# Kernel optimization log

Measured on AMD Instinct MI355X. Metric: run time of the kernel, lower is better.

The kernel has to match this reference:

```python
import jax, jax.numpy as jnp
import numpy as np
import math

S, HID = 2048, 2048
NH, Q_LORA, KV_LORA = 16, 1536, 512
NOPE, ROPE, VDIM = 128, 64, 128
HEAD = NOPE + ROPE  # 192
BLK = 128
EPS = 1e-6
MSCALE = 0.1 * 1.0 * math.log(40.0) + 1.0
SOFTMAX_SCALE = HEAD ** -0.5 * MSCALE * MSCALE


def _dequant(w, s, blk=BLK):
    # w: [out,in] stored quantized values, s: [ceil(out/blk), ceil(in/blk)] block scale_inv
    so = jnp.repeat(s, blk, axis=0)[: w.shape[0]]
    se = jnp.repeat(so, blk, axis=1)[:, : w.shape[1]]
    return w * se


def _mm_dq(x, w, s):
    # mm_w8a16_dq_forward: x @ dequant(w).T
    return x @ _dequant(w, s).T


def _rmsnorm(x, w, eps=EPS):
    var = jnp.mean(x * x, axis=-1, keepdims=True)
    return x * jax.lax.rsqrt(var + eps) * w


def _rotate_half(x):
    h = x.shape[-1] // 2
    return jnp.concatenate([-x[..., h:], x[..., :h]], axis=-1)


def setup_inputs() -> dict:
    key = jax.random.key(0)
    ks = jax.random.split(key, 16)
    d = {
        'hidden_states': jax.random.normal(ks[0], (S, HID), jnp.float32),
        'wq_a': jax.random.normal(ks[1], (Q_LORA, HID), jnp.float32),
        'sq_a': jax.random.uniform(ks[2], (12, 16), jnp.float32) * 0.02 + 0.005,
        'wq_b': jax.random.normal(ks[3], (NH * HEAD, Q_LORA), jnp.float32),
        'sq_b': jax.random.uniform(ks[4], (24, 12), jnp.float32) * 0.02 + 0.005,
        'wkv_a': jax.random.normal(ks[5], (KV_LORA + ROPE, HID), jnp.float32),
        'skv_a': jax.random.uniform(ks[6], (5, 16), jnp.float32) * 0.02 + 0.005,
        'wkv_b': jax.random.normal(ks[7], (NH * (NOPE + VDIM), KV_LORA), jnp.float32),
        'skv_b': jax.random.uniform(ks[8], (32, 4), jnp.float32) * 0.02 + 0.005,
        'wo': jax.random.normal(ks[9], (HID, NH * VDIM), jnp.float32),
        'so': jax.random.uniform(ks[10], (16, 16), jnp.float32) * 0.02 + 0.005,
        'q_ln_w': jnp.ones((Q_LORA,), jnp.float32),
        'kv_ln_w': jnp.ones((KV_LORA,), jnp.float32),
    }
    pos = jnp.arange(S, dtype=jnp.float32)[:, None]
    inv = 1.0 / (10000.0 ** (jnp.arange(0, ROPE, 2, dtype=jnp.float32) / ROPE))
    ang = pos * inv[None, :]
    ang = jnp.concatenate([ang, ang], axis=-1)  # [S, 64]
    d['cos'] = jnp.cos(ang)
    d['sin'] = jnp.sin(ang)
    return d


def reference(hidden_states, cos, sin, wq_a, sq_a, wq_b, sq_b, wkv_a, skv_a,
              wkv_b, skv_b, wo, so, q_ln_w, kv_ln_w):
    # Q low-rank path: q_a -> rmsnorm -> q_b
    lq = _mm_dq(hidden_states, wq_a, sq_a)                 # [S, q_lora]
    q = _mm_dq(_rmsnorm(lq, q_ln_w), wq_b, sq_b)           # [S, NH*HEAD]
    q = q.reshape(S, NH, HEAD)
    q_nope, q_pe = q[..., :NOPE], q[..., NOPE:]            # [S,NH,128], [S,NH,64]

    # KV low-rank + MQA rope path
    lkv = _mm_dq(hidden_states, wkv_a, skv_a)              # [S, kv_lora+rope]
    kv_nope = _rmsnorm(lkv[:, :KV_LORA], kv_ln_w)          # [S, kv_lora]
    k_pe = lkv[:, KV_LORA:]                                # [S, 64] (shared across heads)
    kvb = _mm_dq(kv_nope, wkv_b, skv_b).reshape(S, NH, NOPE + VDIM)
    k_nope, v = kvb[..., :NOPE], kvb[..., NOPE:]           # [S,NH,128] each

    # RoPE (rotate-half) on the pe parts
    q_pe = q_pe * cos[:, None, :] + _rotate_half(q_pe) * sin[:, None, :]
    k_pe = k_pe * cos + _rotate_half(k_pe) * sin           # [S, 64]

    # prefill MLA attention with causal mask
    scores = (jnp.einsum('shd,thd->hst', q_nope, k_nope)
              + jnp.einsum('shd,td->hst', q_pe, k_pe)) * SOFTMAX_SCALE
    causal = jnp.tril(jnp.ones((S, S), bool))
    scores = jnp.where(causal[None], scores, -jnp.inf)
    probs = jax.nn.softmax(scores, axis=-1)                # [NH,S,S]
    attn = jnp.einsum('hst,thd->shd', probs, v).reshape(S, NH * VDIM)

    return _mm_dq(attn, wo, so)                            # [S, HID]
```

## Files before the change

### kernel.cpp

```cpp
#include <hip/hip_runtime.h>

typedef unsigned short u16;
typedef unsigned int u32;
typedef __attribute__((ext_vector_type(8))) short bf16x8;
typedef __attribute__((ext_vector_type(4))) float f32x4;
typedef __attribute__((ext_vector_type(16))) float f32x16;
typedef __attribute__((ext_vector_type(4))) unsigned short u16x4;

#define S_LEN 2048
#define HIDDEN 2048
#define NHEAD 16
#define QLORA 1536
#define KVLORA 512
#define NOPE_D 128
#define ROPE_D 64
#define V_D 128
#define HEAD_D 192
#define NCOMB 2176
#define LOG2E 1.442695041f

__device__ __constant__ float SM_SCALE_C = (float)(0.07216878364870323 *
    ((0.1 * 3.6888794541139363 + 1.0) * (0.1 * 3.6888794541139363 + 1.0)));

__device__ inline u16 f2bf(float f) {
    union { float f; unsigned int u; } v; v.f = f;
    unsigned int r = v.u + 0x7FFFu + ((v.u >> 16) & 1u);
    return (u16)(r >> 16);
}
__device__ inline float bf2f(u16 b) {
    union { unsigned int u; float f; } v; v.u = ((unsigned int)b) << 16;
    return v.f;
}
__device__ inline void gload_lds16(const u16* g, u16* l) {
    __builtin_amdgcn_global_load_lds(
        (const __attribute__((address_space(1))) void*)g,
        (__attribute__((address_space(3))) void*)l, 16, 0, 0);
}

__global__ __launch_bounds__(64)
void prep_weights(const float* __restrict__ hs,
                  const float* __restrict__ wq_a, const float* __restrict__ sq_a,
                  const float* __restrict__ wq_b, const float* __restrict__ sq_b,
                  const float* __restrict__ wkv_a, const float* __restrict__ skv_a,
                  const float* __restrict__ wkv_b, const float* __restrict__ skv_b,
                  const float* __restrict__ wo, const float* __restrict__ so,
                  u16* __restrict__ hs_bf, u16* __restrict__ wcomb,
                  u16* __restrict__ wqb_bf, u16* __restrict__ wkvb_bf,
                  u16* __restrict__ wo_bf) {
    int r = blockIdx.x;
    const float* W; const float* Sc; u16* out; int K, sc_cols, n;
    if (r < 2048)                      { n = r;                     W = hs;    Sc = 0;     out = hs_bf;   K = 2048; sc_cols = 0; }
    else if (r < 2048 + 1536)          { n = r - 2048;              W = wq_a;  Sc = sq_a;  out = wcomb;   K = 2048; sc_cols = 16; }
    else if (r < 2048 + 1536 + 576)    { n = r - (2048 + 1536);     W = wkv_a; Sc = skv_a; out = wcomb + (size_t)QLORA * 2048; K = 2048; sc_cols = 16; }
    else if (r < 2048 + 1536 + 576 + 3072) { n = r - (2048 + 1536 + 576); W = wq_b; Sc = sq_b; out = wqb_bf; K = 1536; sc_cols = 12; }
    else if (r < 2048 + 1536 + 576 + 3072 + 4096) { n = r - (2048 + 1536 + 576 + 3072); W = wkv_b; Sc = skv_b; out = wkvb_bf; K = 512; sc_cols = 4; }
    else                               { n = r - (2048 + 1536 + 576 + 3072 + 4096); W = wo; Sc = so; out = wo_bf; K = 2048; sc_cols = 16; }
    for (int k = threadIdx.x * 8; k < K; k += 512) {
        float sc = Sc ? Sc[(n >> 7) * sc_cols + (k >> 7)] : 1.0f;
        f32x4 v0 = *(const f32x4*)(W + (size_t)n * K + k);
        f32x4 v1 = *(const f32x4*)(W + (size_t)n * K + k + 4);
        bf16x8 o;
        #pragma unroll
        for (int i = 0; i < 4; ++i) {
            o[i]     = (short)f2bf(v0[i] * sc);
            o[i + 4] = (short)f2bf(v1[i] * sc);
        }
        *(bf16x8*)(out + (size_t)n * K + k) = o;
    }
}

__device__ __forceinline__ void gemm_core(
    const u16* __restrict__ A, const u16* __restrict__ W, void* __restrict__ C,
    int M, int N, int Ktot, int Ksub, int mode, int bm, int bn, int bz,
    u16* As, u16* Ws) {
    const int tid = threadIdx.x;
    const int lane = tid & 63;
    const int wv = tid >> 6;
    const int wm = wv >> 1, wn = wv & 1;
    const int lr = lane & 15, lk = lane >> 4;
    const int srow = lane >> 3;
    const int schunk = lane & 7;

    f32x4 acc[4][4] = {};

    const int kbeg = bz * Ksub;
    const int kend = kbeg + Ksub;
    for (int k0 = kbeg; k0 < kend; k0 += 64) {
        __syncthreads();
        #pragma unroll
        for (int i = 0; i < 4; ++i) {
            int t = (wv * 4 + i) * 8 + srow;
            int cs = (schunk ^ (t & 7)) << 3;
            gload_lds16(A + (size_t)(bm + t) * Ktot + k0 + cs, &As[(wv * 4 + i) * 512]);
            gload_lds16(W + (size_t)(bn + t) * Ktot + k0 + cs, &Ws[(wv * 4 + i) * 512]);
        }
        __syncthreads();
        #pragma unroll
        for (int kh = 0; kh < 2; ++kh) {
            bf16x8 af[4], bfr[4];
            #pragma unroll
            for (int mi = 0; mi < 4; ++mi) {
                int r = wm * 64 + mi * 16 + lr;
                af[mi] = *(const bf16x8*)&As[r * 64 + (((kh * 4 + lk) ^ (lr & 7)) << 3)];
            }
            #pragma unroll
            for (int ni = 0; ni < 4; ++ni) {
                int r = wn * 64 + ni * 16 + lr;
                bfr[ni] = *(const bf16x8*)&Ws[r * 64 + (((kh * 4 + lk) ^ (lr & 7)) << 3)];
            }
            #pragma unroll
            for (int mi = 0; mi < 4; ++mi)
                #pragma unroll
                for (int ni = 0; ni < 4; ++ni)
                    acc[mi][ni] = __builtin_amdgcn_mfma_f32_16x16x32_bf16(af[mi], bfr[ni], acc[mi][ni], 0, 0, 0);
        }
    }

    float* Pf = (mode == 2) ? ((float*)C + (size_t)bz * M * N) : (float*)C;
    #pragma unroll
    for (int mi = 0; mi < 4; ++mi)
        #pragma unroll
        for (int ni = 0; ni < 4; ++ni)
            #pragma unroll
            for (int j = 0; j < 4; ++j) {
                int r = bm + wm * 64 + mi * 16 + lk * 4 + j;
                int c = bn + wn * 64 + ni * 16 + lr;
                if (c < N) {
                    if (mode == 1) ((u16*)C)[(size_t)r * N + c] = f2bf(acc[mi][ni][j]);
                    else           Pf[(size_t)r * N + c] = acc[mi][ni][j];
                }
            }
}

__device__ __forceinline__ int xcd_swizzle(int orig, int nwg) {
    int qq = nwg >> 3, rr = nwg & 7, xcd = orig & 7, loc = orig >> 3;
    return (xcd < rr) ? (xcd * (qq + 1) + loc)
                      : (rr * (qq + 1) + (xcd - rr) * qq + loc);
}

__global__ __launch_bounds__(256)
void gemm_bf16(const u16* __restrict__ A, const u16* __restrict__ W,
               void* __restrict__ C, int M, int N, int Ktot, int Ksub, int mode) {
    __shared__ u16 As[128 * 64];
    __shared__ u16 Ws[128 * 64];
    const int gx = gridDim.x, gy = gridDim.y;
    const int nwg = gx * gy * gridDim.z;
    const int orig = blockIdx.x + gx * (blockIdx.y + gy * blockIdx.z);
    const int wg = xcd_swizzle(orig, nwg);
    const int bn = (wg % gx) * 128;
    const int bm = ((wg / gx) % gy) * 128;
    const int bz = wg / (gx * gy);
    gemm_core(A, W, C, M, N, Ktot, Ksub, mode, bm, bn, bz, As, Ws);
}

__global__ __launch_bounds__(256)
void gemm_qh_kvb(const u16* __restrict__ lqn, const u16* __restrict__ wqb, float* __restrict__ arena,
                 const u16* __restrict__ kvn, const u16* __restrict__ wkvb, u16* __restrict__ kvb) {
    __shared__ u16 As[128 * 64];
    __shared__ u16 Ws[128 * 64];
    const int NWG = 24 * 16 * 3 + 32 * 16;
    const int wg = xcd_swizzle(blockIdx.x, NWG);
    if (wg < 24 * 16 * 3) {
        const int bn = (wg % 24) * 128;
        const int bm = ((wg / 24) % 16) * 128;
        const int bz = wg / (24 * 16);
        gemm_core(lqn, wqb, arena, S_LEN, NHEAD * HEAD_D, QLORA, 512, 2, bm, bn, bz, As, Ws);
    } else {
        const int w2 = wg - 24 * 16 * 3;
        const int bn = (w2 % 32) * 128;
        const int bm = (w2 / 32) * 128;
        gemm_core(kvn, wkvb, kvb, S_LEN, NHEAD * 256, KVLORA, 512, 1, bm, bn, 0, As, Ws);
    }
}

__global__ __launch_bounds__(256)
void reduce_rms_comb(const float* __restrict__ P,
                     const float* __restrict__ q_ln, const float* __restrict__ kv_ln,
                     u16* __restrict__ lqn, u16* __restrict__ kvn, u16* __restrict__ kpe) {
    __shared__ float vbuf[NCOMB];
    __shared__ float r2[2][4];
    const int row = blockIdx.x;
    const float* p0 = P + (size_t)row * NCOMB;
    const size_t st = (size_t)S_LEN * NCOMB;
    float ssq = 0.f, ssk = 0.f;
    for (int c = threadIdx.x * 4; c < NCOMB; c += 1024) {
        f32x4 v = *(const f32x4*)(p0 + c);
        v += *(const f32x4*)(p0 + st + c);
        v += *(const f32x4*)(p0 + 2 * st + c);
        v += *(const f32x4*)(p0 + 3 * st + c);
        *(f32x4*)&vbuf[c] = v;
        float s = v[0] * v[0] + v[1] * v[1] + v[2] * v[2] + v[3] * v[3];
        if (c < QLORA) ssq += s;
        else if (c < QLORA + KVLORA) ssk += s;
    }
    #pragma unroll
    for (int off = 1; off < 64; off <<= 1) {
        ssq += __shfl_xor(ssq, off, 64);
        ssk += __shfl_xor(ssk, off, 64);
    }
    if ((threadIdx.x & 63) == 0) {
        r2[0][threadIdx.x >> 6] = ssq;
        r2[1][threadIdx.x >> 6] = ssk;
    }
    __syncthreads();
    float rsq = rsqrtf((r2[0][0] + r2[0][1] + r2[0][2] + r2[0][3]) / (float)QLORA + 1e-6f);
    float rsk = rsqrtf((r2[1][0] + r2[1][1] + r2[1][2] + r2[1][3]) / (float)KVLORA + 1e-6f);
    for (int c = threadIdx.x * 4; c < NCOMB; c += 1024) {
        f32x4 v = *(const f32x4*)&vbuf[c];
        u16x4 o;
        if (c < QLORA) {
            #pragma unroll
            for (int j = 0; j < 4; ++j) o[j] = f2bf(v[j] * rsq * q_ln[c + j]);
            *(u16x4*)(lqn + (size_t)row * QLORA + c) = o;
        } else if (c < QLORA + KVLORA) {
            int cc = c - QLORA;
            #pragma unroll
            for (int j = 0; j < 4; ++j) o[j] = f2bf(v[j] * rsk * kv_ln[cc + j]);
            *(u16x4*)(kvn + (size_t)row * KVLORA + cc) = o;
        } else if (c < QLORA + KVLORA + ROPE_D) {
            int cc = c - QLORA - KVLORA;
            #pragma unroll
            for (int j = 0; j < 4; ++j) o[j] = f2bf(v[j]);
            *(u16x4*)(kpe + (size_t)row * ROPE_D + cc) = o;
        }
    }
}

__global__ __launch_bounds__(256)
void prep_q_frag_red(const float* __restrict__ P, const float* __restrict__ cosb,
                     const float* __restrict__ sinb, u16* __restrict__ qfrag) {
    const int sblk = blockIdx.x, h = blockIdx.y;
    const float sm = SM_SCALE_C;
    const size_t st = (size_t)S_LEN * (NHEAD * HEAD_D);
    #pragma unroll
    for (int c = 0; c < 3; ++c) {
        int idx = c * 256 + threadIdx.x;
        int kk = idx >> 6;
        int lane = idx & 63;
        int s = sblk * 32 + (lane & 31);
        int d0 = kk * 16 + (lane >> 5) * 8;
        const float* p0 = P + (size_t)s * (NHEAD * HEAD_D) + h * HEAD_D;
        bf16x8 o;
        if (d0 < NOPE_D) {
            f32x4 a0 = *(const f32x4*)(p0 + d0) + *(const f32x4*)(p0 + st + d0) + *(const f32x4*)(p0 + 2 * st + d0);
            f32x4 a1 = *(const f32x4*)(p0 + d0 + 4) + *(const f32x4*)(p0 + st + d0 + 4) + *(const f32x4*)(p0 + 2 * st + d0 + 4);
            #pragma unroll
            for (int j = 0; j < 4; ++j) {
                o[j]     = (short)f2bf(a0[j] * sm);
                o[j + 4] = (short)f2bf(a1[j] * sm);
            }
        } else {
            int r0 = d0 - NOPE_D;
            int rp = (r0 + 32) & 63;
            f32x4 x0 = *(const f32x4*)(p0 + d0) + *(const f32x4*)(p0 + st + d0) + *(const f32x4*)(p0 + 2 * st + d0);
            f32x4 x1 = *(const f32x4*)(p0 + d0 + 4) + *(const f32x4*)(p0 + st + d0 + 4) + *(const f32x4*)(p0 + 2 * st + d0 + 4);
            f32x4 r0v = *(const f32x4*)(p0 + NOPE_D + rp) + *(const f32x4*)(p0 + st + NOPE_D + rp) + *(const f32x4*)(p0 + 2 * st + NOPE_D + rp);
            f32x4 r1v = *(const f32x4*)(p0 + NOPE_D + rp + 4) + *(const f32x4*)(p0 + st + NOPE_D + rp + 4) + *(const f32x4*)(p0 + 2 * st + NOPE_D + rp + 4);
            float x[8], rv[8];
            #pragma unroll
            for (int j = 0; j < 4; ++j) { x[j] = x0[j]; x[j + 4] = x1[j]; rv[j] = r0v[j]; rv[j + 4] = r1v[j]; }
            float sign = (r0 < 32) ? -1.f : 1.f;
            #pragma unroll
            for (int j = 0; j < 8; ++j) {
                float cs = cosb[s * ROPE_D + r0 + j];
                float sn = sinb[s * ROPE_D + r0 + j];
                o[j] = (short)f2bf((x[j] * cs + sign * rv[j] * sn) * sm);
            }
        }
        *(bf16x8*)(qfrag + (((size_t)h * 64 + sblk) * 12 + kk) * 512 + lane * 8) = o;
    }
}

__global__ void reduce_out(const float* __restrict__ P, float* __restrict__ out, int n) {
    int i = (blockIdx.x * blockDim.x + threadIdx.x) * 4;
    if (i >= n) return;
    f32x4 v = *(const f32x4*)(P + i);
    v += *(const f32x4*)(P + (size_t)n + i);
    v += *(const f32x4*)(P + 2 * (size_t)n + i);
    v += *(const f32x4*)(P + 3 * (size_t)n + i);
    *(f32x4*)(out + i) = v;
}

__global__ __launch_bounds__(256)
void prep_kv_frag(const u16* __restrict__ kvb, const u16* __restrict__ kpe,
                  const float* __restrict__ cosb, const float* __restrict__ sinb,
                  u16* __restrict__ kfrag, u16* __restrict__ vfrag) {
    __shared__ u16 Vs[32][136];
    const int sblk = blockIdx.x, h = blockIdx.y;
    #pragma unroll
    for (int it = 0; it < 2; ++it) {
        int idx = it * 256 + threadIdx.x;
        int r = idx >> 4;
        int c8 = (idx & 15) * 8;
        int s = sblk * 32 + r;
        *(bf16x8*)&Vs[r][c8] = *(const bf16x8*)(kvb + (size_t)s * (NHEAD * 256) + h * 256 + NOPE_D + c8);
    }
    #pragma unroll
    for (int c = 0; c < 3; ++c) {
        int idx = c * 256 + threadIdx.x;
        int kk = idx >> 6;
        int lane = idx & 63;
        int s = sblk * 32 + (lane & 31);
        int d0 = kk * 16 + (lane >> 5) * 8;
        bf16x8 o;
        if (d0 < NOPE_D) {
            o = *(const bf16x8*)(kvb + (size_t)s * (NHEAD * 256) + h * 256 + d0);
        } else {
            int r0 = d0 - NOPE_D;
            const u16* kp = kpe + (size_t)s * ROPE_D;
            bf16x8 x = *(const bf16x8*)(kp + r0);
            bf16x8 rv = *(const bf16x8*)(kp + ((r0 + 32) & 63));
            float sign = (r0 < 32) ? -1.f : 1.f;
            #pragma unroll
            for (int j = 0; j < 8; ++j) {
                float cs = cosb[s * ROPE_D + r0 + j];
                float sn = sinb[s * ROPE_D + r0 + j];
                o[j] = (short)f2bf(bf2f((u16)x[j]) * cs + sign * bf2f((u16)rv[j]) * sn);
            }
        }
        *(bf16x8*)(kfrag + (((size_t)h * 64 + sblk) * 12 + kk) * 512 + lane * 8) = o;
    }
    __syncthreads();
    #pragma unroll
    for (int it = 0; it < 2; ++it) {
        int idx = it * 256 + threadIdx.x;
        int fi = idx >> 6;
        int lane = idx & 63;
        int bb = fi >> 1, h16 = fi & 1;
        int col = bb * 32 + (lane & 31);
        int row0 = h16 * 16 + (lane >> 5) * 8;
        bf16x8 o;
        #pragma unroll
        for (int j = 0; j < 8; ++j) o[j] = (short)Vs[row0 + j][col];
        *(bf16x8*)(vfrag + (((size_t)h * 64 + sblk) * 8 + fi) * 512 + lane * 8) = o;
    }
}

__global__ __launch_bounds__(256, 2)
void flash_attn4(const u16* __restrict__ qfrag, const u16* __restrict__ kfrag,
                 const u16* __restrict__ vfrag, u16* __restrict__ attn) {
    __shared__ float OB[3][128][32];
    __shared__ float MB[3][2][32];

    const int tid = threadIdx.x, lane = tid & 63, wq = tid >> 6;
    const int b = blockIdx.x;
    const int t = 63 - (b >> 4);
    const int h = ((b & 7) << 1) | ((b >> 3) & 1);
    const int q0 = t * 32;
    const int lq = lane & 31;
    const int hi = lane >> 5;

    const int n = t + 1;
    const int s_lo = (wq * n) >> 2;
    const int s_hi = ((wq + 1) * n) >> 2;

    bf16x8 qfr[12];
    {
        const u16* qb = qfrag + (((size_t)h * 64 + t) * 12) * 512 + lane * 8;
        #pragma unroll
        for (int kk = 0; kk < 12; ++kk) qfr[kk] = *(const bf16x8*)(qb + kk * 512);
    }

    const u16* kfb = kfrag + ((size_t)h * 64 * 12) * 512 + lane * 8;
    const u16* vfb = vfrag + ((size_t)h * 64 * 8) * 512 + lane * 8;

    f32x16 oa[4] = {};
    float mrun = -3.0e38f, lrun = 0.f;

    bf16x8 kcur[12];
    {
        int psub = (s_lo < s_hi) ? s_lo : 0;
        const u16* kp = kfb + (size_t)psub * 12 * 512;
        #pragma unroll
        for (int kk = 0; kk < 12; ++kk)
            kcur[kk] = *(const bf16x8*)(kp + kk * 512);
    }

    for (int sub = s_lo; sub < s_hi; ++sub) {
        f32x16 s0 = {}, s1 = {};
        __builtin_amdgcn_s_setprio(1);
        #pragma unroll
        for (int kk = 0; kk < 12; kk += 2) {
            s0 = __builtin_amdgcn_mfma_f32_32x32x16_bf16(kcur[kk], qfr[kk], s0, 0, 0, 0);
            s1 = __builtin_amdgcn_mfma_f32_32x32x16_bf16(kcur[kk + 1], qfr[kk + 1], s1, 0, 0, 0);
        }
        __builtin_amdgcn_s_setprio(0);
        {
            int nsub = (sub + 1 < s_hi) ? sub + 1 : sub;
            const u16* kp = kfb + (size_t)nsub * 12 * 512;
            #pragma unroll
            for (int kk = 0; kk < 12; ++kk)
                kcur[kk] = *(const bf16x8*)(kp + kk * 512);
        }
        bf16x8 va[8];
        {
            const u16* vp = vfb + (size_t)sub * 8 * 512;
            #pragma unroll
            for (int fi = 0; fi < 8; ++fi)
                va[fi] = *(const bf16x8*)(vp + fi * 512);
        }
        f32x16 sv = s0 + s1;
        if (sub == t) {
            #pragma unroll
            for (int r = 0; r < 16; ++r) {
                int krow = (r & 3) + 8 * (r >> 2) + 4 * hi;
                if (krow > lq) sv[r] = -3.0e38f;
            }
        }
        float tm = sv[0];
        #pragma unroll
        for (int r = 1; r < 16; ++r) tm = fmaxf(tm, sv[r]);
        tm = fmaxf(tm, __shfl_xor(tm, 32, 64));
        if (!__all(tm - mrun <= 8.f)) {
            float mn = fmaxf(mrun, tm);
            float scl = exp2f((mrun - mn) * LOG2E);
            mrun = mn;
            lrun *= scl;
            #pragma unroll
            for (int bb = 0; bb < 4; ++bb)
                #pragma unroll
                for (int r = 0; r < 16; ++r) oa[bb][r] *= scl;
        }
        float p[16];
        float psum = 0.f;
        #pragma unroll
        for (int r = 0; r < 16; ++r) {
            p[r] = exp2f((sv[r] - mrun) * LOG2E);
            psum += p[r];
        }
        psum += __shfl_xor(psum, 32, 64);
        lrun += psum;
        u32 pw[8], sw[8];
        #pragma unroll
        for (int i = 0; i < 8; ++i)
            pw[i] = (u32)f2bf(p[2 * i]) | ((u32)f2bf(p[2 * i + 1]) << 16);
        #pragma unroll
        for (int i = 0; i < 8; ++i)
            sw[i] = (u32)__shfl_xor((int)pw[i], 32, 64);
        union { u32 w[4]; bf16x8 v; } bf0, bf1;
        bf0.w[0] = hi ? sw[2] : pw[0];
        bf0.w[1] = hi ? sw[3] : pw[1];
        bf0.w[2] = hi ? pw[2] : sw[0];
        bf0.w[3] = hi ? pw[3] : sw[1];
        bf1.w[0] = hi ? sw[6] : pw[4];
        bf1.w[1] = hi ? sw[7] : pw[5];
        bf1.w[2] = hi ? pw[6] : sw[4];
        bf1.w[3] = hi ? pw[7] : sw[5];
        __builtin_amdgcn_s_setprio(1);
        #pragma unroll
        for (int bb = 0; bb < 4; ++bb) {
            oa[bb] = __builtin_amdgcn_mfma_f32_32x32x16_bf16(va[bb * 2],     bf0.v, oa[bb], 0, 0, 0);
            oa[bb] = __builtin_amdgcn_mfma_f32_32x32x16_bf16(va[bb * 2 + 1], bf1.v, oa[bb], 0, 0, 0);
        }
        __builtin_amdgcn_s_setprio(0);
    }

    if (wq) {
        #pragma unroll
        for (int bb = 0; bb < 4; ++bb)
            #pragma unroll
            for (int r = 0; r < 16; ++r) {
                int dv = bb * 32 + (r & 3) + 8 * (r >> 2) + 4 * hi;
                OB[wq - 1][dv][lq] = oa[bb][r];
            }
        if (lane < 32) {
            MB[wq - 1][0][lane] = mrun;
            MB[wq - 1][1][lane] = lrun;
        }
    }
    __syncthreads();
    if (!wq) {
        float m1 = MB[0][0][lq], l1 = MB[0][1][lq];
        float m2 = MB[1][0][lq], l2 = MB[1][1][lq];
        float m3 = MB[2][0][lq], l3 = MB[2][1][lq];
        float M = fmaxf(fmaxf(mrun, m1), fmaxf(m2, m3));
        float e0 = exp2f((mrun - M) * LOG2E);
        float e1 = exp2f((m1 - M) * LOG2E);
        float e2 = exp2f((m2 - M) * LOG2E);
        float e3 = exp2f((m3 - M) * LOG2E);
        float L = lrun * e0 + l1 * e1 + l2 * e2 + l3 * e3;
        float inv = 1.0f / L;
        u16* ob = attn + (size_t)(q0 + lq) * (NHEAD * V_D) + h * V_D;
        #pragma unroll
        for (int bb = 0; bb < 4; ++bb)
            #pragma unroll
            for (int rq = 0; rq < 4; ++rq) {
                u16x4 pk;
                #pragma unroll
                for (int rb = 0; rb < 4; ++rb) {
                    int r = rq * 4 + rb;
                    int dv = bb * 32 + rb + 8 * rq + 4 * hi;
                    float o = (oa[bb][r] * e0 + OB[0][dv][lq] * e1 +
                               OB[1][dv][lq] * e2 + OB[2][dv][lq] * e3) * inv;
                    pk[rb] = f2bf(o);
                }
                *(u16x4*)(ob + bb * 32 + 8 * rq + 4 * hi) = pk;
            }
    }
}

extern "C" void kernel_launch(void* const* d_in, const int* in_sizes, int n_in,
                              void* d_out, int out_size, void* d_ws, size_t ws_size,
                              hipStream_t stream) {
    const float* hs    = (const float*)d_in[0];
    const float* wq_a  = (const float*)d_in[1];
    const float* sq_a  = (const float*)d_in[2];
    const float* wq_b  = (const float*)d_in[3];
    const float* sq_b  = (const float*)d_in[4];
    const float* wkv_a = (const float*)d_in[5];
    const float* skv_a = (const float*)d_in[6];
    const float* wkv_b = (const float*)d_in[7];
    const float* skv_b = (const float*)d_in[8];
    const float* wo    = (const float*)d_in[9];
    const float* so    = (const float*)d_in[10];
    const float* q_ln  = (const float*)d_in[11];
    const float* kv_ln = (const float*)d_in[12];
    const float* cosb  = (const float*)d_in[13];
    const float* sinb  = (const float*)d_in[14];
    float* out = (float*)d_out;

    char* ws = (char*)d_ws;
    size_t off = 0;
    auto alloc = [&](size_t bytes) -> void* {
        void* p = ws + off; off += (bytes + 255) & ~(size_t)255; return p;
    };
    u16* hs_bf  = (u16*)alloc((size_t)S_LEN * HIDDEN * 2);
    u16* lqn    = (u16*)alloc((size_t)S_LEN * QLORA * 2);
    u16* kvn    = (u16*)alloc((size_t)S_LEN * KVLORA * 2);
    u16* kpe    = (u16*)alloc((size_t)S_LEN * ROPE_D * 2);
    u16* kvb    = (u16*)alloc((size_t)S_LEN * NHEAD * 256 * 2);
    u16* attn   = (u16*)alloc((size_t)S_LEN * NHEAD * V_D * 2);
    u16* qfrag  = (u16*)alloc((size_t)NHEAD * 64 * 12 * 512 * 2);
    u16* kfrag  = (u16*)alloc((size_t)NHEAD * 64 * 12 * 512 * 2);
    u16* vfrag  = (u16*)alloc((size_t)NHEAD * 64 * 8 * 512 * 2);
    u16* wcomb  = (u16*)alloc((size_t)NCOMB * HIDDEN * 2);
    u16* wqb_bf  = (u16*)alloc((size_t)(NHEAD * HEAD_D) * QLORA * 2);
    u16* wkvb_bf = (u16*)alloc((size_t)(NHEAD * 256) * KVLORA * 2);
    u16* wo_bf   = (u16*)alloc((size_t)HIDDEN * (NHEAD * V_D) * 2);
    float* arena = (float*)alloc((size_t)3 * S_LEN * (NHEAD * HEAD_D) * 4);

    prep_weights<<<2048 + 1536 + 576 + 3072 + 4096 + 2048, 64, 0, stream>>>(
        hs, wq_a, sq_a, wq_b, sq_b, wkv_a, skv_a, wkv_b, skv_b, wo, so,
        hs_bf, wcomb, wqb_bf, wkvb_bf, wo_bf);

    gemm_bf16<<<dim3(NCOMB / 128, S_LEN / 128, 4), 256, 0, stream>>>(hs_bf, wcomb, arena,
        S_LEN, NCOMB, HIDDEN, HIDDEN / 4, 2);
    reduce_rms_comb<<<S_LEN, 256, 0, stream>>>(arena, q_ln, kv_ln, lqn, kvn, kpe);

    gemm_qh_kvb<<<24 * 16 * 3 + 32 * 16, 256, 0, stream>>>(lqn, wqb_bf, arena, kvn, wkvb_bf, kvb);
    prep_q_frag_red<<<dim3(64, NHEAD), 256, 0, stream>>>(arena, cosb, sinb, qfrag);

    prep_kv_frag<<<dim3(64, NHEAD), 256, 0, stream>>>(kvb, kpe, cosb, sinb, kfrag, vfrag);

    flash_attn4<<<1024, 256, 0, stream>>>(qfrag, kfrag, vfrag, attn);

    gemm_bf16<<<dim3(HIDDEN / 128, S_LEN / 128, 4), 256, 0, stream>>>(attn, wo_bf, arena,
        S_LEN, HIDDEN, NHEAD * V_D, (NHEAD * V_D) / 4, 2);
    reduce_out<<<(S_LEN * HIDDEN / 4 + 255) / 256, 256, 0, stream>>>(arena, out, S_LEN * HIDDEN);
}
```

Baseline: 239.8 us.

## Store split-K partials as bf16 and fuse weight prep into GEMM and frag kernels

Split-K GEMM partial sums are now written as bf16 instead of fp32, halving partial-buffer traffic in the GEMMs and in the reduce kernels. Weight dequantisation is split: the first-stage weights and hidden states are converted in a wider-block kernel, and the remaining weight conversions run as extra workgroups inside the first GEMM launch to overlap with it. The Q and KV fragment preparation kernels are merged into one launch with a z-dimension. Rounding the partials to bf16 before summing adds accuracy loss on the output and intermediates.

```diff
diff --git a/kernel.cpp b/kernel.cpp
--- a/kernel.cpp
+++ b/kernel.cpp
@@ -36,42 +36,29 @@
         (const __attribute__((address_space(1))) void*)g,
         (__attribute__((address_space(3))) void*)l, 16, 0, 0);
 }
-
-__global__ __launch_bounds__(64)
-void prep_weights(const float* __restrict__ hs,
-                  const float* __restrict__ wq_a, const float* __restrict__ sq_a,
-                  const float* __restrict__ wq_b, const float* __restrict__ sq_b,
-                  const float* __restrict__ wkv_a, const float* __restrict__ skv_a,
-                  const float* __restrict__ wkv_b, const float* __restrict__ skv_b,
-                  const float* __restrict__ wo, const float* __restrict__ so,
-                  u16* __restrict__ hs_bf, u16* __restrict__ wcomb,
-                  u16* __restrict__ wqb_bf, u16* __restrict__ wkvb_bf,
-                  u16* __restrict__ wo_bf) {
-    int r = blockIdx.x;
-    const float* W; const float* Sc; u16* out; int K, sc_cols, n;
-    if (r < 2048)                      { n = r;                     W = hs;    Sc = 0;     out = hs_bf;   K = 2048; sc_cols = 0; }
-    else if (r < 2048 + 1536)          { n = r - 2048;              W = wq_a;  Sc = sq_a;  out = wcomb;   K = 2048; sc_cols = 16; }
-    else if (r < 2048 + 1536 + 576)    { n = r - (2048 + 1536);     W = wkv_a; Sc = skv_a; out = wcomb + (size_t)QLORA * 2048; K = 2048; sc_cols = 16; }
-    else if (r < 2048 + 1536 + 576 + 3072) { n = r - (2048 + 1536 + 576); W = wq_b; Sc = sq_b; out = wqb_bf; K = 1536; sc_cols = 12; }
-    else if (r < 2048 + 1536 + 576 + 3072 + 4096) { n = r - (2048 + 1536 + 576 + 3072); W = wkv_b; Sc = skv_b; out = wkvb_bf; K = 512; sc_cols = 4; }
-    else                               { n = r - (2048 + 1536 + 576 + 3072 + 4096); W = wo; Sc = so; out = wo_bf; K = 2048; sc_cols = 16; }
-    for (int k = threadIdx.x * 8; k < K; k += 512) {
-        float sc = Sc ? Sc[(n >> 7) * sc_cols + (k >> 7)] : 1.0f;
-        f32x4 v0 = *(const f32x4*)(W + (size_t)n * K + k);
-        f32x4 v1 = *(const f32x4*)(W + (size_t)n * K + k + 4);
-        bf16x8 o;
-        #pragma unroll
-        for (int i = 0; i < 4; ++i) {
-            o[i]     = (short)f2bf(v0[i] * sc);
-            o[i + 4] = (short)f2bf(v1[i] * sc);
-        }
-        *(bf16x8*)(out + (size_t)n * K + k) = o;
-    }
+__device__ __forceinline__ void dequant_row8(const float* __restrict__ W, const float* __restrict__ Sc,
+                                             u16* __restrict__ out, int n, int K, int sc_cols, int k) {
+    float sc = Sc ? Sc[(n >> 7) * sc_cols + (k >> 7)] : 1.0f;
+    f32x4 v0 = *(const f32x4*)(W + (size_t)n * K + k);
+    f32x4 v1 = *(const f32x4*)(W + (size_t)n * K + k + 4);
+    bf16x8 o;
+    #pragma unroll
+    for (int i = 0; i < 4; ++i) {
+        o[i]     = (short)f2bf(v0[i] * sc);
+        o[i + 4] = (short)f2bf(v1[i] * sc);
+    }
+    *(bf16x8*)(out + (size_t)n * K + k) = o;
+}
+
+__device__ __forceinline__ int xcd_swizzle(int orig, int nwg) {
+    int qq = nwg >> 3, rr = nwg & 7, xcd = orig & 7, loc = orig >> 3;
+    return (xcd < rr) ? (xcd * (qq + 1) + loc)
+                      : (rr * (qq + 1) + (xcd - rr) * qq + loc);
 }
 
 __device__ __forceinline__ void gemm_core(
-    const u16* __restrict__ A, const u16* __restrict__ W, void* __restrict__ C,
-    int M, int N, int Ktot, int Ksub, int mode, int bm, int bn, int bz,
+    const u16* __restrict__ A, const u16* __restrict__ W, u16* __restrict__ C,
+    int M, int N, int Ktot, int Ksub, int bm, int bn, int bz,
     u16* As, u16* Ws) {
     const int tid = threadIdx.x;
     const int lane = tid & 63;
@@ -116,7 +103,7 @@
         }
     }
 
-    float* Pf = (mode == 2) ? ((float*)C + (size_t)bz * M * N) : (float*)C;
+    u16* Pb = C + (size_t)bz * M * N;
     #pragma unroll
     for (int mi = 0; mi < 4; ++mi)
         #pragma unroll
@@ -125,22 +112,56 @@
             for (int j = 0; j < 4; ++j) {
                 int r = bm + wm * 64 + mi * 16 + lk * 4 + j;
                 int c = bn + wn * 64 + ni * 16 + lr;
-                if (c < N) {
-                    if (mode == 1) ((u16*)C)[(size_t)r * N + c] = f2bf(acc[mi][ni][j]);
-                    else           Pf[(size_t)r * N + c] = acc[mi][ni][j];
-                }
-            }
-}
-
-__device__ __forceinline__ int xcd_swizzle(int orig, int nwg) {
-    int qq = nwg >> 3, rr = nwg & 7, xcd = orig & 7, loc = orig >> 3;
-    return (xcd < rr) ? (xcd * (qq + 1) + loc)
-                      : (rr * (qq + 1) + (xcd - rr) * qq + loc);
+                if (c < N) Pb[(size_t)r * N + c] = f2bf(acc[mi][ni][j]);
+            }
+}
+
+__global__ __launch_bounds__(256)
+void prep_weights_a(const float* __restrict__ hs,
+                    const float* __restrict__ wq_a, const float* __restrict__ sq_a,
+                    const float* __restrict__ wkv_a, const float* __restrict__ skv_a,
+                    u16* __restrict__ hs_bf, u16* __restrict__ wcomb) {
+    int r = blockIdx.x * 4 + (threadIdx.x >> 6);
+    const float* W; const float* Sc; u16* out; int n, sc_cols;
+    if (r < 2048)      { W = hs;    Sc = 0;      out = hs_bf; n = r;        sc_cols = 0; }
+    else if (r < 3584) { W = wq_a;  Sc = sq_a;   out = wcomb; n = r - 2048; sc_cols = 16; }
+    else               { W = wkv_a; Sc = skv_a;  out = wcomb + (size_t)QLORA * 2048; n = r - 3584; sc_cols = 16; }
+    for (int k = (threadIdx.x & 63) * 8; k < 2048; k += 512)
+        dequant_row8(W, Sc, out, n, 2048, sc_cols, k);
+}
+
+__global__ __launch_bounds__(256)
+void gemm_comb_prepw(const u16* __restrict__ hs_bf, const u16* __restrict__ wcomb,
+                     u16* __restrict__ arena,
+                     const float* __restrict__ wq_b, const float* __restrict__ sq_b,
+                     const float* __restrict__ wkv_b, const float* __restrict__ skv_b,
+                     const float* __restrict__ wo, const float* __restrict__ so,
+                     u16* __restrict__ wqb_bf, u16* __restrict__ wkvb_bf,
+                     u16* __restrict__ wo_bf) {
+    __shared__ u16 As[128 * 64];
+    __shared__ u16 Ws[128 * 64];
+    const int NWG = 17 * 16 * 4 + 2304;
+    const int wg = xcd_swizzle(blockIdx.x, NWG);
+    if (wg < 17 * 16 * 4) {
+        const int bn = (wg % 17) * 128;
+        const int bm = ((wg / 17) % 16) * 128;
+        const int bz = wg / (17 * 16);
+        gemm_core(hs_bf, wcomb, arena, S_LEN, NCOMB, HIDDEN, HIDDEN / 4, bm, bn, bz, As, Ws);
+    } else {
+        const int w2 = wg - 17 * 16 * 4;
+        int r = w2 * 4 + (threadIdx.x >> 6);
+        const float* W; const float* Sc; u16* out; int n, K, sc_cols;
+        if (r < 3072)      { W = wq_b;  Sc = sq_b;  out = wqb_bf;  n = r;        K = 1536; sc_cols = 12; }
+        else if (r < 7168) { W = wkv_b; Sc = skv_b; out = wkvb_bf; n = r - 3072; K = 512;  sc_cols = 4; }
+        else               { W = wo;    Sc = so;    out = wo_bf;   n = r - 7168; K = 2048; sc_cols = 16; }
+        for (int k = (threadIdx.x & 63) * 8; k < K; k += 512)
+            dequant_row8(W, Sc, out, n, K, sc_cols, k);
+    }
 }
 
 __global__ __launch_bounds__(256)
 void gemm_bf16(const u16* __restrict__ A, const u16* __restrict__ W,
-               void* __restrict__ C, int M, int N, int Ktot, int Ksub, int mode) {
+               u16* __restrict__ C, int M, int N, int Ktot, int Ksub) {
     __shared__ u16 As[128 * 64];
     __shared__ u16 Ws[128 * 64];
     const int gx = gridDim.x, gy = gridDim.y;
@@ -150,11 +171,11 @@
     const int bn = (wg % gx) * 128;
     const int bm = ((wg / gx) % gy) * 128;
     const int bz = wg / (gx * gy);
-    gemm_core(A, W, C, M, N, Ktot, Ksub, mode, bm, bn, bz, As, Ws);
+    gemm_core(A, W, C, M, N, Ktot, Ksub, bm, bn, bz, As, Ws);
 }
 
 __global__ __launch_bounds__(256)
-void gemm_qh_kvb(const u16* __restrict__ lqn, const u16* __restrict__ wqb, float* __restrict__ arena,
+void gemm_qh_kvb(const u16* __restrict__ lqn, const u16* __restrict__ wqb, u16* __restrict__ arena,
                  const u16* __restrict__ kvn, const u16* __restrict__ wkvb, u16* __restrict__ kvb) {
     __shared__ u16 As[128 * 64];
     __shared__ u16 Ws[128 * 64];
@@ -164,32 +185,37 @@
         const int bn = (wg % 24) * 128;
         const int bm = ((wg / 24) % 16) * 128;
         const int bz = wg / (24 * 16);
-        gemm_core(lqn, wqb, arena, S_LEN, NHEAD * HEAD_D, QLORA, 512, 2, bm, bn, bz, As, Ws);
+        gemm_core(lqn, wqb, arena, S_LEN, NHEAD * HEAD_D, QLORA, 512, bm, bn, bz, As, Ws);
     } else {
         const int w2 = wg - 24 * 16 * 3;
         const int bn = (w2 % 32) * 128;
         const int bm = (w2 / 32) * 128;
-        gemm_core(kvn, wkvb, kvb, S_LEN, NHEAD * 256, KVLORA, 512, 1, bm, bn, 0, As, Ws);
+        gemm_core(kvn, wkvb, kvb, S_LEN, NHEAD * 256, KVLORA, 512, bm, bn, 0, As, Ws);
     }
 }
 
 __global__ __launch_bounds__(256)
-void reduce_rms_comb(const float* __restrict__ P,
+void reduce_rms_comb(const u16* __restrict__ P,
                      const float* __restrict__ q_ln, const float* __restrict__ kv_ln,
                      u16* __restrict__ lqn, u16* __restrict__ kvn, u16* __restrict__ kpe) {
     __shared__ float vbuf[NCOMB];
     __shared__ float r2[2][4];
     const int row = blockIdx.x;
-    const float* p0 = P + (size_t)row * NCOMB;
+    const u16* p0 = P + (size_t)row * NCOMB;
     const size_t st = (size_t)S_LEN * NCOMB;
     float ssq = 0.f, ssk = 0.f;
-    for (int c = threadIdx.x * 4; c < NCOMB; c += 1024) {
-        f32x4 v = *(const f32x4*)(p0 + c);
-        v += *(const f32x4*)(p0 + st + c);
-        v += *(const f32x4*)(p0 + 2 * st + c);
-        v += *(const f32x4*)(p0 + 3 * st + c);
-        *(f32x4*)&vbuf[c] = v;
-        float s = v[0] * v[0] + v[1] * v[1] + v[2] * v[2] + v[3] * v[3];
+    for (int c = threadIdx.x * 8; c < NCOMB; c += 2048) {
+        bf16x8 a0 = *(const bf16x8*)(p0 + c);
+        bf16x8 a1 = *(const bf16x8*)(p0 + st + c);
+        bf16x8 a2 = *(const bf16x8*)(p0 + 2 * st + c);
+        bf16x8 a3 = *(const bf16x8*)(p0 + 3 * st + c);
+        float s = 0.f;
+        #pragma unroll
+        for (int j = 0; j < 8; ++j) {
+            float v = bf2f((u16)a0[j]) + bf2f((u16)a1[j]) + bf2f((u16)a2[j]) + bf2f((u16)a3[j]);
+            vbuf[c + j] = v;
+            s += v * v;
+        }
         if (c < QLORA) ssq += s;
         else if (c < QLORA + KVLORA) ssk += s;
     }
@@ -205,135 +231,143 @@
     __syncthreads();
     float rsq = rsqrtf((r2[0][0] + r2[0][1] + r2[0][2] + r2[0][3]) / (float)QLORA + 1e-6f);
     float rsk = rsqrtf((r2[1][0] + r2[1][1] + r2[1][2] + r2[1][3]) / (float)KVLORA + 1e-6f);
-    for (int c = threadIdx.x * 4; c < NCOMB; c += 1024) {
-        f32x4 v = *(const f32x4*)&vbuf[c];
-        u16x4 o;
+    for (int c = threadIdx.x * 8; c < NCOMB; c += 2048) {
+        bf16x8 o;
         if (c < QLORA) {
             #pragma unroll
-            for (int j = 0; j < 4; ++j) o[j] = f2bf(v[j] * rsq * q_ln[c + j]);
-            *(u16x4*)(lqn + (size_t)row * QLORA + c) = o;
+            for (int j = 0; j < 8; ++j) o[j] = (short)f2bf(vbuf[c + j] * rsq * q_ln[c + j]);
+            *(bf16x8*)(lqn + (size_t)row * QLORA + c) = o;
         } else if (c < QLORA + KVLORA) {
             int cc = c - QLORA;
             #pragma unroll
-            for (int j = 0; j < 4; ++j) o[j] = f2bf(v[j] * rsk * kv_ln[cc + j]);
-            *(u16x4*)(kvn + (size_t)row * KVLORA + cc) = o;
+            for (int j = 0; j < 8; ++j) o[j] = (short)f2bf(vbuf[c + j] * rsk * kv_ln[cc + j]);
+            *(bf16x8*)(kvn + (size_t)row * KVLORA + cc) = o;
         } else if (c < QLORA + KVLORA + ROPE_D) {
             int cc = c - QLORA - KVLORA;
             #pragma unroll
-            for (int j = 0; j < 4; ++j) o[j] = f2bf(v[j]);
-            *(u16x4*)(kpe + (size_t)row * ROPE_D + cc) = o;
+            for (int j = 0; j < 8; ++j) o[j] = (short)f2bf(vbuf[c + j]);
+            *(bf16x8*)(kpe + (size_t)row * ROPE_D + cc) = o;
         }
     }
 }
 
 __global__ __launch_bounds__(256)
-void prep_q_frag_red(const float* __restrict__ P, const float* __restrict__ cosb,
-                     const float* __restrict__ sinb, u16* __restrict__ qfrag) {
-    const int sblk = blockIdx.x, h = blockIdx.y;
-    const float sm = SM_SCALE_C;
-    const size_t st = (size_t)S_LEN * (NHEAD * HEAD_D);
-    #pragma unroll
-    for (int c = 0; c < 3; ++c) {
-        int idx = c * 256 + threadIdx.x;
-        int kk = idx >> 6;
-        int lane = idx & 63;
-        int s = sblk * 32 + (lane & 31);
-        int d0 = kk * 16 + (lane >> 5) * 8;
-        const float* p0 = P + (size_t)s * (NHEAD * HEAD_D) + h * HEAD_D;
-        bf16x8 o;
-        if (d0 < NOPE_D) {
-            f32x4 a0 = *(const f32x4*)(p0 + d0) + *(const f32x4*)(p0 + st + d0) + *(const f32x4*)(p0 + 2 * st + d0);
-            f32x4 a1 = *(const f32x4*)(p0 + d0 + 4) + *(const f32x4*)(p0 + st + d0 + 4) + *(const f32x4*)(p0 + 2 * st + d0 + 4);
-            #pragma unroll
-            for (int j = 0; j < 4; ++j) {
-                o[j]     = (short)f2bf(a0[j] * sm);
-                o[j + 4] = (short)f2bf(a1[j] * sm);
-            }
-        } else {
-            int r0 = d0 - NOPE_D;
-            int rp = (r0 + 32) & 63;
-            f32x4 x0 = *(const f32x4*)(p0 + d0) + *(const f32x4*)(p0 + st + d0) + *(const f32x4*)(p0 + 2 * st + d0);
-            f32x4 x1 = *(const f32x4*)(p0 + d0 + 4) + *(const f32x4*)(p0 + st + d0 + 4) + *(const f32x4*)(p0 + 2 * st + d0 + 4);
-            f32x4 r0v = *(const f32x4*)(p0 + NOPE_D + rp) + *(const f32x4*)(p0 + st + NOPE_D + rp) + *(const f32x4*)(p0 + 2 * st + NOPE_D + rp);
-            f32x4 r1v = *(const f32x4*)(p0 + NOPE_D + rp + 4) + *(const f32x4*)(p0 + st + NOPE_D + rp + 4) + *(const f32x4*)(p0 + 2 * st + NOPE_D + rp + 4);
-            float x[8], rv[8];
-            #pragma unroll
-            for (int j = 0; j < 4; ++j) { x[j] = x0[j]; x[j + 4] = x1[j]; rv[j] = r0v[j]; rv[j + 4] = r1v[j]; }
-            float sign = (r0 < 32) ? -1.f : 1.f;
-            #pragma unroll
-            for (int j = 0; j < 8; ++j) {
-                float cs = cosb[s * ROPE_D + r0 + j];
-                float sn = sinb[s * ROPE_D + r0 + j];
-                o[j] = (short)f2bf((x[j] * cs + sign * rv[j] * sn) * sm);
-            }
-        }
-        *(bf16x8*)(qfrag + (((size_t)h * 64 + sblk) * 12 + kk) * 512 + lane * 8) = o;
-    }
-}
-
-__global__ void reduce_out(const float* __restrict__ P, float* __restrict__ out, int n) {
-    int i = (blockIdx.x * blockDim.x + threadIdx.x) * 4;
-    if (i >= n) return;
-    f32x4 v = *(const f32x4*)(P + i);
-    v += *(const f32x4*)(P + (size_t)n + i);
-    v += *(const f32x4*)(P + 2 * (size_t)n + i);
-    v += *(const f32x4*)(P + 3 * (size_t)n + i);
-    *(f32x4*)(out + i) = v;
-}
-
-__global__ __launch_bounds__(256)
-void prep_kv_frag(const u16* __restrict__ kvb, const u16* __restrict__ kpe,
-                  const float* __restrict__ cosb, const float* __restrict__ sinb,
-                  u16* __restrict__ kfrag, u16* __restrict__ vfrag) {
+void prep_qkv_frag(const u16* __restrict__ P, const u16* __restrict__ kvb,
+                   const u16* __restrict__ kpe, const float* __restrict__ cosb,
+                   const float* __restrict__ sinb, u16* __restrict__ qfrag,
+                   u16* __restrict__ kfrag, u16* __restrict__ vfrag) {
     __shared__ u16 Vs[32][136];
     const int sblk = blockIdx.x, h = blockIdx.y;
+    if (blockIdx.z == 0) {
+        const float sm = SM_SCALE_C;
+        const size_t st = (size_t)S_LEN * (NHEAD * HEAD_D);
+        #pragma unroll
+        for (int c = 0; c < 3; ++c) {
+            int idx = c * 256 + threadIdx.x;
+            int kk = idx >> 6;
+            int lane = idx & 63;
+            int s = sblk * 32 + (lane & 31);
+            int d0 = kk * 16 + (lane >> 5) * 8;
+            const u16* p0 = P + (size_t)s * (NHEAD * HEAD_D) + h * HEAD_D;
+            float x[8];
+            {
+                bf16x8 a0 = *(const bf16x8*)(p0 + d0);
+                bf16x8 a1 = *(const bf16x8*)(p0 + st + d0);
+                bf16x8 a2 = *(const bf16x8*)(p0 + 2 * st + d0);
+                #pragma unroll
+                for (int j = 0; j < 8; ++j)
+                    x[j] = bf2f((u16)a0[j]) + bf2f((u16)a1[j]) + bf2f((u16)a2[j]);
+            }
+            bf16x8 o;
+            if (d0 < NOPE_D) {
+                #pragma unroll
+                for (int j = 0; j < 8; ++j) o[j] = (short)f2bf(x[j] * sm);
+            } else {
+                int r0 = d0 - NOPE_D;
+                int rp = (r0 + 32) & 63;
+                float rv[8];
+                bf16x8 b0 = *(const bf16x8*)(p0 + NOPE_D + rp);
+                bf16x8 b1 = *(const bf16x8*)(p0 + st + NOPE_D + rp);
+                bf16x8 b2 = *(const bf16x8*)(p0 + 2 * st + NOPE_D + rp);
+                #pragma unroll
+                for (int j = 0; j < 8; ++j)
+                    rv[j] = bf2f((u16)b0[j]) + bf2f((u16)b1[j]) + bf2f((u16)b2[j]);
+                float sign = (r0 < 32) ? -1.f : 1.f;
+                #pragma unroll
+                for (int j = 0; j < 8; ++j) {
+                    float cs = cosb[s * ROPE_D + r0 + j];
+                    float sn = sinb[s * ROPE_D + r0 + j];
+                    o[j] = (short)f2bf((x[j] * cs + sign * rv[j] * sn) * sm);
+                }
+            }
+            *(bf16x8*)(qfrag + (((size_t)h * 64 + sblk) * 12 + kk) * 512 + lane * 8) = o;
+        }
+    } else {
+        #pragma unroll
+        for (int it = 0; it < 2; ++it) {
+            int idx = it * 256 + threadIdx.x;
+            int r = idx >> 4;
+            int c8 = (idx & 15) * 8;
+            int s = sblk * 32 + r;
+            *(bf16x8*)&Vs[r][c8] = *(const bf16x8*)(kvb + (size_t)s * (NHEAD * 256) + h * 256 + NOPE_D + c8);
+        }
+        #pragma unroll
+        for (int c = 0; c < 3; ++c) {
+            int idx = c * 256 + threadIdx.x;
+            int kk = idx >> 6;
+            int lane = idx & 63;
+            int s = sblk * 32 + (lane & 31);
+            int d0 = kk * 16 + (lane >> 5) * 8;
+            bf16x8 o;
+            if (d0 < NOPE_D) {
+                o = *(const bf16x8*)(kvb + (size_t)s * (NHEAD * 256) + h * 256 + d0);
+            } else {
+                int r0 = d0 - NOPE_D;
+                const u16* kp = kpe + (size_t)s * ROPE_D;
+                bf16x8 x = *(const bf16x8*)(kp + r0);
+                bf16x8 rv = *(const bf16x8*)(kp + ((r0 + 32) & 63));
+                float sign = (r0 < 32) ? -1.f : 1.f;
+                #pragma unroll
+                for (int j = 0; j < 8; ++j) {
+                    float cs = cosb[s * ROPE_D + r0 + j];
+                    float sn = sinb[s * ROPE_D + r0 + j];
+                    o[j] = (short)f2bf(bf2f((u16)x[j]) * cs + sign * bf2f((u16)rv[j]) * sn);
+                }
+            }
+            *(bf16x8*)(kfrag + (((size_t)h * 64 + sblk) * 12 + kk) * 512 + lane * 8) = o;
+        }
+        __syncthreads();
+        #pragma unroll
+        for (int it = 0; it < 2; ++it) {
+            int idx = it * 256 + threadIdx.x;
+            int fi = idx >> 6;
+            int lane = idx & 63;
+            int bb = fi >> 1, h16 = fi & 1;
+            int col = bb * 32 + (lane & 31);
+            int row0 = h16 * 16 + (lane >> 5) * 8;
+            bf16x8 o;
+            #pragma unroll
+            for (int j = 0; j < 8; ++j) o[j] = (short)Vs[row0 + j][col];
+            *(bf16x8*)(vfrag + (((size_t)h * 64 + sblk) * 8 + fi) * 512 + lane * 8) = o;
+        }
+    }
+}
+
+__global__ void reduce_out(const u16* __restrict__ P, float* __restrict__ out, int n) {
+    int i = (blockIdx.x * blockDim.x + threadIdx.x) * 8;
+    if (i >= n) return;
+    bf16x8 a0 = *(const bf16x8*)(P + i);
+    bf16x8 a1 = *(const bf16x8*)(P + (size_t)n + i);
+    bf16x8 a2 = *(const bf16x8*)(P + 2 * (size_t)n + i);
+    bf16x8 a3 = *(const bf16x8*)(P + 3 * (size_t)n + i);
+    f32x4 o0, o1;
     #pragma unroll
-    for (int it = 0; it < 2; ++it) {
-        int idx = it * 256 + threadIdx.x;
-        int r = idx >> 4;
-        int c8 = (idx & 15) * 8;
-        int s = sblk * 32 + r;
-        *(bf16x8*)&Vs[r][c8] = *(const bf16x8*)(kvb + (size_t)s * (NHEAD * 256) + h * 256 + NOPE_D + c8);
-    }
-    #pragma unroll
-    for (int c = 0; c < 3; ++c) {
-        int idx = c * 256 + threadIdx.x;
-        int kk = idx >> 6;
-        int lane = idx & 63;
-        int s = sblk * 32 + (lane & 31);
-        int d0 = kk * 16 + (lane >> 5) * 8;
-        bf16x8 o;
-        if (d0 < NOPE_D) {
-            o = *(const bf16x8*)(kvb + (size_t)s * (NHEAD * 256) + h * 256 + d0);
-        } else {
-            int r0 = d0 - NOPE_D;
-            const u16* kp = kpe + (size_t)s * ROPE_D;
-            bf16x8 x = *(const bf16x8*)(kp + r0);
-            bf16x8 rv = *(const bf16x8*)(kp + ((r0 + 32) & 63));
-            float sign = (r0 < 32) ? -1.f : 1.f;
-            #pragma unroll
-            for (int j = 0; j < 8; ++j) {
-                float cs = cosb[s * ROPE_D + r0 + j];
-                float sn = sinb[s * ROPE_D + r0 + j];
-                o[j] = (short)f2bf(bf2f((u16)x[j]) * cs + sign * bf2f((u16)rv[j]) * sn);
-            }
-        }
-        *(bf16x8*)(kfrag + (((size_t)h * 64 + sblk) * 12 + kk) * 512 + lane * 8) = o;
-    }
-    __syncthreads();
-    #pragma unroll
-    for (int it = 0; it < 2; ++it) {
-        int idx = it * 256 + threadIdx.x;
-        int fi = idx >> 6;
-        int lane = idx & 63;
-        int bb = fi >> 1, h16 = fi & 1;
-        int col = bb * 32 + (lane & 31);
-        int row0 = h16 * 16 + (lane >> 5) * 8;
-        bf16x8 o;
-        #pragma unroll
-        for (int j = 0; j < 8; ++j) o[j] = (short)Vs[row0 + j][col];
-        *(bf16x8*)(vfrag + (((size_t)h * 64 + sblk) * 8 + fi) * 512 + lane * 8) = o;
-    }
+    for (int j = 0; j < 4; ++j) {
+        o0[j] = bf2f((u16)a0[j]) + bf2f((u16)a1[j]) + bf2f((u16)a2[j]) + bf2f((u16)a3[j]);
+        o1[j] = bf2f((u16)a0[j + 4]) + bf2f((u16)a1[j + 4]) + bf2f((u16)a2[j + 4]) + bf2f((u16)a3[j + 4]);
+    }
+    *(f32x4*)(out + i) = o0;
+    *(f32x4*)(out + i + 4) = o1;
 }
 
 __global__ __launch_bounds__(256, 2)
@@ -537,24 +571,22 @@
     u16* wqb_bf  = (u16*)alloc((size_t)(NHEAD * HEAD_D) * QLORA * 2);
     u16* wkvb_bf = (u16*)alloc((size_t)(NHEAD * 256) * KVLORA * 2);
     u16* wo_bf   = (u16*)alloc((size_t)HIDDEN * (NHEAD * V_D) * 2);
-    float* arena = (float*)alloc((size_t)3 * S_LEN * (NHEAD * HEAD_D) * 4);
-
-    prep_weights<<<2048 + 1536 + 576 + 3072 + 4096 + 2048, 64, 0, stream>>>(
-        hs, wq_a, sq_a, wq_b, sq_b, wkv_a, skv_a, wkv_b, skv_b, wo, so,
-        hs_bf, wcomb, wqb_bf, wkvb_bf, wo_bf);
-
-    gemm_bf16<<<dim3(NCOMB / 128, S_LEN / 128, 4), 256, 0, stream>>>(hs_bf, wcomb, arena,
-        S_LEN, NCOMB, HIDDEN, HIDDEN / 4, 2);
+    u16* arena  = (u16*)alloc((size_t)4 * S_LEN * NCOMB * 2);
+
+    prep_weights_a<<<1040, 256, 0, stream>>>(hs, wq_a, sq_a, wkv_a, skv_a, hs_bf, wcomb);
+
+    gemm_comb_prepw<<<3392, 256, 0, stream>>>(hs_bf, wcomb, arena,
+        wq_b, sq_b, wkv_b, skv_b, wo, so, wqb_bf, wkvb_bf, wo_bf);
     reduce_rms_comb<<<S_LEN, 256, 0, stream>>>(arena, q_ln, kv_ln, lqn, kvn, kpe);
 
     gemm_qh_kvb<<<24 * 16 * 3 + 32 * 16, 256, 0, stream>>>(lqn, wqb_bf, arena, kvn, wkvb_bf, kvb);
-    prep_q_frag_red<<<dim3(64, NHEAD), 256, 0, stream>>>(arena, cosb, sinb, qfrag);
-
-    prep_kv_frag<<<dim3(64, NHEAD), 256, 0, stream>>>(kvb, kpe, cosb, sinb, kfrag, vfrag);
+
+    prep_qkv_frag<<<dim3(64, NHEAD, 2), 256, 0, stream>>>(arena, kvb, kpe, cosb, sinb,
+        qfrag, kfrag, vfrag);
 
     flash_attn4<<<1024, 256, 0, stream>>>(qfrag, kfrag, vfrag, attn);
 
-    gemm_bf16<<<dim3(HIDDEN / 128, S_LEN / 128, 4), 256, 0, stream>>>(attn, wo_bf, arena,
-        S_LEN, HIDDEN, NHEAD * V_D, (NHEAD * V_D) / 4, 2);
-    reduce_out<<<(S_LEN * HIDDEN / 4 + 255) / 256, 256, 0, stream>>>(arena, out, S_LEN * HIDDEN);
-}
+    gemm_bf16<<<dim3(16, 16, 4), 256, 0, stream>>>(attn, wo_bf, arena,
+        S_LEN, HIDDEN, NHEAD * V_D, (NHEAD * V_D) / 4);
+    reduce_out<<<S_LEN * HIDDEN / 8 / 256, 256, 0, stream>>>(arena, out, S_LEN * HIDDEN);
+}
```

Measured after the change: 224.1 us. 1.07x faster.
